# Optimization experiments

Hardware: AMD Instinct MI355X
Metric: run time of the kernel (lower is better)

The kernel has to match this reference:

```python
import jax, jax.numpy as jnp
import numpy as np

N = 50000       # nodes
E = 800000      # edges (avg degree 16)
DIN = 128
DOUT = 128
ALPHA = 0.2     # leaky relu negative slope


def setup_inputs() -> dict:
    key = jax.random.key(0)
    k1, k2, k3, k4, k5 = jax.random.split(key, 5)
    h = jax.random.normal(k1, (N, DIN), dtype=jnp.float32)
    # xavier-normal-ish scaling for params
    W = jax.random.normal(k2, (DIN, DOUT), dtype=jnp.float32) * np.float32(np.sqrt(2.0 / (DIN + DOUT)))
    a = jax.random.normal(k3, (2 * DOUT,), dtype=jnp.float32) * np.float32(np.sqrt(2.0 / (2 * DOUT + 1)))
    src = jax.random.randint(k4, (E,), 0, N, dtype=jnp.int32)
    dst = jax.random.randint(k5, (E,), 0, N, dtype=jnp.int32)
    return {"h": h, "W": W, "a": a, "src": src, "dst": dst}


def reference(h, W, a, src, dst):
    # eval mode: dropout is a no-op (training=False)
    Wh = h @ W                                  # [N, DOUT]
    a_src, a_dst = a[:DOUT], a[DOUT:]
    s = Wh @ a_src                              # [N] per-node src score
    d = Wh @ a_dst                              # [N] per-node dst score
    e = jax.nn.leaky_relu(s[src] + d[dst], negative_slope=ALPHA)  # [E]
    # segment softmax over incoming edges of each dst node
    emax = jax.ops.segment_max(e, dst, num_segments=N)            # [N]
    emax = jnp.where(jnp.isfinite(emax), emax, jnp.float32(0.0))  # isolated nodes
    ex = jnp.exp(e - emax[dst])                                   # [E]
    denom = jax.ops.segment_sum(ex, dst, num_segments=N)          # [N]
    alpha = ex / denom[dst]                                       # [E]
    # weighted scatter-sum of src features into dst nodes
    h_out = jax.ops.segment_sum(alpha[:, None] * Wh[src], dst, num_segments=N)  # [N, DOUT]
    # residual: in_feats == out_feats -> Identity
    return h_out + h
```

## Files before the change

kernel.cpp:

```cpp
#include <hip/hip_runtime.h>
#include <math.h>

#define NN 50000
#define NE 800000
#define DD 128
#define LRELU 0.2f
#define CAP 64

typedef unsigned int uint;

__device__ __forceinline__ uint pack_bf2(float x, float y) {
  uint a = __float_as_uint(x), b = __float_as_uint(y);
  a = (a + 0x7fffu + ((a >> 16) & 1u)) >> 16;
  b = (b + 0x7fffu + ((b >> 16) & 1u)) >> 16;
  return a | (b << 16);
}

__global__ __launch_bounds__(256) void k_gemm(const float* __restrict__ h,
                                              const float* __restrict__ W,
                                              const float* __restrict__ a,
                                              uint* __restrict__ Whb,
                                              float* __restrict__ sv,
                                              float* __restrict__ dv,
                                              int* __restrict__ cnt) {
  __shared__ float hs[32][64];
  __shared__ float Ws[32][128];
  const int tid = threadIdx.x;
  const int brow = blockIdx.x * 64;

  if (tid < 64) {
    int idx = blockIdx.x * 64 + tid;
    if (idx < NN) cnt[idx] = 0;
  }

  const int tx = tid & 15, ty = tid >> 4;
  const int c0 = tx * 4, c1 = 64 + tx * 4;
  float acc[4][8];
#pragma unroll
  for (int r = 0; r < 4; ++r)
#pragma unroll
    for (int j = 0; j < 8; ++j) acc[r][j] = 0.f;

  const int lr = tid >> 2;
  const int lc = (tid & 3) * 8;
  int grow = brow + lr; if (grow >= NN) grow = 0;

  for (int k0 = 0; k0 < DD; k0 += 32) {
    {
      const float4* hp = reinterpret_cast<const float4*>(h + (size_t)grow * DD + k0 + lc);
      float4 v0 = hp[0], v1 = hp[1];
      hs[lc + 0][lr] = v0.x; hs[lc + 1][lr] = v0.y;
      hs[lc + 2][lr] = v0.z; hs[lc + 3][lr] = v0.w;
      hs[lc + 4][lr] = v1.x; hs[lc + 5][lr] = v1.y;
      hs[lc + 6][lr] = v1.z; hs[lc + 7][lr] = v1.w;
    }
#pragma unroll
    for (int i = 0; i < 4; ++i) {
      int f = i * 256 + tid;
      int kk = f >> 5, cc = (f & 31) * 4;
      *reinterpret_cast<float4*>(&Ws[kk][cc]) =
          *reinterpret_cast<const float4*>(W + (size_t)(k0 + kk) * DD + cc);
    }
    __syncthreads();
#pragma unroll
    for (int k = 0; k < 32; ++k) {
      float4 av = *reinterpret_cast<const float4*>(&hs[k][ty * 4]);
      float4 b0 = *reinterpret_cast<const float4*>(&Ws[k][c0]);
      float4 b1 = *reinterpret_cast<const float4*>(&Ws[k][c1]);
      acc[0][0] = fmaf(av.x, b0.x, acc[0][0]); acc[0][1] = fmaf(av.x, b0.y, acc[0][1]);
      acc[0][2] = fmaf(av.x, b0.z, acc[0][2]); acc[0][3] = fmaf(av.x, b0.w, acc[0][3]);
      acc[0][4] = fmaf(av.x, b1.x, acc[0][4]); acc[0][5] = fmaf(av.x, b1.y, acc[0][5]);
      acc[0][6] = fmaf(av.x, b1.z, acc[0][6]); acc[0][7] = fmaf(av.x, b1.w, acc[0][7]);
      acc[1][0] = fmaf(av.y, b0.x, acc[1][0]); acc[1][1] = fmaf(av.y, b0.y, acc[1][1]);
      acc[1][2] = fmaf(av.y, b0.z, acc[1][2]); acc[1][3] = fmaf(av.y, b0.w, acc[1][3]);
      acc[1][4] = fmaf(av.y, b1.x, acc[1][4]); acc[1][5] = fmaf(av.y, b1.y, acc[1][5]);
      acc[1][6] = fmaf(av.y, b1.z, acc[1][6]); acc[1][7] = fmaf(av.y, b1.w, acc[1][7]);
      acc[2][0] = fmaf(av.z, b0.x, acc[2][0]); acc[2][1] = fmaf(av.z, b0.y, acc[2][1]);
      acc[2][2] = fmaf(av.z, b0.z, acc[2][2]); acc[2][3] = fmaf(av.z, b0.w, acc[2][3]);
      acc[2][4] = fmaf(av.z, b1.x, acc[2][4]); acc[2][5] = fmaf(av.z, b1.y, acc[2][5]);
      acc[2][6] = fmaf(av.z, b1.z, acc[2][6]); acc[2][7] = fmaf(av.z, b1.w, acc[2][7]);
      acc[3][0] = fmaf(av.w, b0.x, acc[3][0]); acc[3][1] = fmaf(av.w, b0.y, acc[3][1]);
      acc[3][2] = fmaf(av.w, b0.z, acc[3][2]); acc[3][3] = fmaf(av.w, b0.w, acc[3][3]);
      acc[3][4] = fmaf(av.w, b1.x, acc[3][4]); acc[3][5] = fmaf(av.w, b1.y, acc[3][5]);
      acc[3][6] = fmaf(av.w, b1.z, acc[3][6]); acc[3][7] = fmaf(av.w, b1.w, acc[3][7]);
    }
    __syncthreads();
  }

  float4 as0 = *reinterpret_cast<const float4*>(a + c0);
  float4 as1 = *reinterpret_cast<const float4*>(a + c1);
  float4 ad0 = *reinterpret_cast<const float4*>(a + DD + c0);
  float4 ad1 = *reinterpret_cast<const float4*>(a + DD + c1);
#pragma unroll
  for (int r = 0; r < 4; ++r) {
    int row = brow + ty * 4 + r;
    bool ok = row < NN;
    if (ok) {
      uint2 p0 = make_uint2(pack_bf2(acc[r][0], acc[r][1]), pack_bf2(acc[r][2], acc[r][3]));
      uint2 p1 = make_uint2(pack_bf2(acc[r][4], acc[r][5]), pack_bf2(acc[r][6], acc[r][7]));
      *reinterpret_cast<uint2*>(Whb + (size_t)row * 64 + c0 / 2) = p0;
      *reinterpret_cast<uint2*>(Whb + (size_t)row * 64 + c1 / 2) = p1;
    }
    float ps = acc[r][0] * as0.x + acc[r][1] * as0.y + acc[r][2] * as0.z + acc[r][3] * as0.w
             + acc[r][4] * as1.x + acc[r][5] * as1.y + acc[r][6] * as1.z + acc[r][7] * as1.w;
    float pd = acc[r][0] * ad0.x + acc[r][1] * ad0.y + acc[r][2] * ad0.z + acc[r][3] * ad0.w
             + acc[r][4] * ad1.x + acc[r][5] * ad1.y + acc[r][6] * ad1.z + acc[r][7] * ad1.w;
#pragma unroll
    for (int off = 8; off > 0; off >>= 1) {
      ps += __shfl_xor(ps, off);
      pd += __shfl_xor(pd, off);
    }
    if (tx == 0 && ok) { sv[row] = ps; dv[row] = pd; }
  }
}

__global__ __launch_bounds__(256) void k_fill(const int* __restrict__ src,
                                              const int* __restrict__ dst,
                                              int* __restrict__ cnt,
                                              int* __restrict__ srcs) {
  int i = blockIdx.x * 256 + threadIdx.x;
  if (i >= NE) return;
  int d = dst[i];
  int p = atomicAdd(&cnt[d], 1);
  if (p < CAP) srcs[(size_t)d * CAP + p] = src[i];
}

__global__ __launch_bounds__(256) void k_node(const float* __restrict__ h,
                                              const uint* __restrict__ Whb,
                                              const float* __restrict__ sv,
                                              const float* __restrict__ dv,
                                              const int* __restrict__ cnt,
                                              const int* __restrict__ srcs,
                                              float* __restrict__ out) {
  int wid = (blockIdx.x * 256 + threadIdx.x) >> 6;
  if (wid >= NN) return;
  wid = __builtin_amdgcn_readfirstlane(wid);
  const int lane = threadIdx.x & 63;

  float2 hrow = reinterpret_cast<const float2*>(h + (size_t)wid * DD)[lane];
  int deg = cnt[wid];
  deg = deg < CAP ? deg : CAP;
  float2* o2 = reinterpret_cast<float2*>(out + (size_t)wid * DD);
  if (deg == 0) { o2[lane] = hrow; return; }

  const int* bucket = srcs + (size_t)wid * CAP;
  const float dvn = dv[wid];

  float m = -INFINITY;
  for (int k = lane; k < deg; k += 64) {
    float ev = sv[bucket[k]] + dvn;
    ev = ev > 0.f ? ev : LRELU * ev;
    m = fmaxf(m, ev);
  }
#pragma unroll
  for (int off = 32; off > 0; off >>= 1) m = fmaxf(m, __shfl_xor(m, off));

  float2 accA = make_float2(0.f, 0.f);
  float2 accB = make_float2(0.f, 0.f);
  float den = 0.f;
  int k = 0;
  for (; k + 2 <= deg; k += 2) {
    int s0 = bucket[k], s1 = bucket[k + 1];
    float e0 = sv[s0] + dvn; e0 = e0 > 0.f ? e0 : LRELU * e0;
    float e1 = sv[s1] + dvn; e1 = e1 > 0.f ? e1 : LRELU * e1;
    float x0 = __expf(e0 - m), x1 = __expf(e1 - m);
    den += x0 + x1;
    uint u0 = Whb[(size_t)s0 * 64 + lane];
    uint u1 = Whb[(size_t)s1 * 64 + lane];
    accA.x = fmaf(x0, __uint_as_float(u0 << 16), accA.x);
    accA.y = fmaf(x0, __uint_as_float(u0 & 0xffff0000u), accA.y);
    accB.x = fmaf(x1, __uint_as_float(u1 << 16), accB.x);
    accB.y = fmaf(x1, __uint_as_float(u1 & 0xffff0000u), accB.y);
  }
  if (k < deg) {
    int s0 = bucket[k];
    float e0 = sv[s0] + dvn; e0 = e0 > 0.f ? e0 : LRELU * e0;
    float x0 = __expf(e0 - m);
    den += x0;
    uint u0 = Whb[(size_t)s0 * 64 + lane];
    accA.x = fmaf(x0, __uint_as_float(u0 << 16), accA.x);
    accA.y = fmaf(x0, __uint_as_float(u0 & 0xffff0000u), accA.y);
  }
  float inv = 1.0f / den;
  o2[lane] = make_float2(hrow.x + (accA.x + accB.x) * inv,
                         hrow.y + (accA.y + accB.y) * inv);
}

extern "C" void kernel_launch(void* const* d_in, const int* in_sizes, int n_in,
                              void* d_out, int out_size, void* d_ws, size_t ws_size,
                              hipStream_t stream) {
  const float* h = (const float*)d_in[0];
  const float* W = (const float*)d_in[1];
  const float* a = (const float*)d_in[2];
  const int* src = (const int*)d_in[3];
  const int* dst = (const int*)d_in[4];
  float* out = (float*)d_out;

  char* ws = (char*)d_ws;
  uint*  Whb = (uint*) (ws);
  float* sv  = (float*)(ws + 12800000);
  float* dv  = (float*)(ws + 13000000);
  int*   cnt = (int*)  (ws + 13200000);
  int*   srcs= (int*)  (ws + 13400000);

  hipLaunchKernelGGL(k_gemm, dim3((NN + 63) / 64), dim3(256), 0, stream,
                     h, W, a, Whb, sv, dv, cnt);
  hipLaunchKernelGGL(k_fill, dim3((NE + 255) / 256), dim3(256), 0, stream,
                     src, dst, cnt, srcs);
  hipLaunchKernelGGL(k_node, dim3((NN + 3) / 4), dim3(256), 0, stream,
                     h, Whb, sv, dv, cnt, srcs, out);
}
```

Measured before the change: 201.1 us.

## Precompute edge exp weights in fill and partition nodes by XCD slice

The fill kernel now computes each edge's LeakyReLU score and its exponential, and stores (src, weight) pairs in the per-node buckets. The node kernel therefore no longer does the gather-based max pass or the exp work. Both the fill and node kernels split destination nodes into 8 slices keyed on blockIdx&7, so that the atomics, bucket writes and later reads for a node tend to stay within one XCD's L2. In exchange, every fill block scans its edge range 8 times, the bucket entries double in size, and dropping the max subtraction risks exp overflow on inputs with large scores.

```diff
diff --git a/kernel.cpp b/kernel.cpp
--- a/kernel.cpp
+++ b/kernel.cpp
@@ -6,6 +6,7 @@
 #define DD 128
 #define LRELU 0.2f
 #define CAP 64
+#define SLICE 6256
 
 typedef unsigned int uint;
 
@@ -116,24 +117,34 @@
 
 __global__ __launch_bounds__(256) void k_fill(const int* __restrict__ src,
                                               const int* __restrict__ dst,
+                                              const float* __restrict__ sv,
+                                              const float* __restrict__ dv,
                                               int* __restrict__ cnt,
-                                              int* __restrict__ srcs) {
-  int i = blockIdx.x * 256 + threadIdx.x;
-  if (i >= NE) return;
-  int d = dst[i];
-  int p = atomicAdd(&cnt[d], 1);
-  if (p < CAP) srcs[(size_t)d * CAP + p] = src[i];
+                                              uint2* __restrict__ entries) {
+  const int xcd = blockIdx.x & 7;
+  const int e0 = (blockIdx.x >> 3) * 3125;
+  const int e1 = e0 + 3125;
+  for (int i = e0 + threadIdx.x; i < e1; i += 256) {
+    int d = dst[i];
+    if (d / SLICE != xcd) continue;
+    int s = src[i];
+    float ev = sv[s] + dv[d];
+    ev = ev > 0.f ? ev : LRELU * ev;
+    float x = __expf(ev);
+    int p = atomicAdd(&cnt[d], 1);
+    if (p < CAP) entries[(size_t)d * CAP + p] = make_uint2((uint)s, __float_as_uint(x));
+  }
 }
 
 __global__ __launch_bounds__(256) void k_node(const float* __restrict__ h,
                                               const uint* __restrict__ Whb,
-                                              const float* __restrict__ sv,
-                                              const float* __restrict__ dv,
                                               const int* __restrict__ cnt,
-                                              const int* __restrict__ srcs,
+                                              const uint2* __restrict__ entries,
                                               float* __restrict__ out) {
-  int wid = (blockIdx.x * 256 + threadIdx.x) >> 6;
-  if (wid >= NN) return;
+  const int sl = blockIdx.x & 7;
+  int wid = sl * SLICE + (blockIdx.x >> 3) * 4 + (threadIdx.x >> 6);
+  const int lim = min(NN, (sl + 1) * SLICE);
+  if (wid >= lim) return;
   wid = __builtin_amdgcn_readfirstlane(wid);
   const int lane = threadIdx.x & 63;
 
@@ -143,41 +154,27 @@
   float2* o2 = reinterpret_cast<float2*>(out + (size_t)wid * DD);
   if (deg == 0) { o2[lane] = hrow; return; }
 
-  const int* bucket = srcs + (size_t)wid * CAP;
-  const float dvn = dv[wid];
-
-  float m = -INFINITY;
-  for (int k = lane; k < deg; k += 64) {
-    float ev = sv[bucket[k]] + dvn;
-    ev = ev > 0.f ? ev : LRELU * ev;
-    m = fmaxf(m, ev);
-  }
-#pragma unroll
-  for (int off = 32; off > 0; off >>= 1) m = fmaxf(m, __shfl_xor(m, off));
-
+  const uint2* bucket = entries + (size_t)wid * CAP;
   float2 accA = make_float2(0.f, 0.f);
   float2 accB = make_float2(0.f, 0.f);
   float den = 0.f;
   int k = 0;
   for (; k + 2 <= deg; k += 2) {
-    int s0 = bucket[k], s1 = bucket[k + 1];
-    float e0 = sv[s0] + dvn; e0 = e0 > 0.f ? e0 : LRELU * e0;
-    float e1 = sv[s1] + dvn; e1 = e1 > 0.f ? e1 : LRELU * e1;
-    float x0 = __expf(e0 - m), x1 = __expf(e1 - m);
+    uint2 q0 = bucket[k], q1 = bucket[k + 1];
+    float x0 = __uint_as_float(q0.y), x1 = __uint_as_float(q1.y);
     den += x0 + x1;
-    uint u0 = Whb[(size_t)s0 * 64 + lane];
-    uint u1 = Whb[(size_t)s1 * 64 + lane];
+    uint u0 = Whb[(size_t)q0.x * 64 + lane];
+    uint u1 = Whb[(size_t)q1.x * 64 + lane];
     accA.x = fmaf(x0, __uint_as_float(u0 << 16), accA.x);
     accA.y = fmaf(x0, __uint_as_float(u0 & 0xffff0000u), accA.y);
     accB.x = fmaf(x1, __uint_as_float(u1 << 16), accB.x);
     accB.y = fmaf(x1, __uint_as_float(u1 & 0xffff0000u), accB.y);
   }
   if (k < deg) {
-    int s0 = bucket[k];
-    float e0 = sv[s0] + dvn; e0 = e0 > 0.f ? e0 : LRELU * e0;
-    float x0 = __expf(e0 - m);
+    uint2 q0 = bucket[k];
+    float x0 = __uint_as_float(q0.y);
     den += x0;
-    uint u0 = Whb[(size_t)s0 * 64 + lane];
+    uint u0 = Whb[(size_t)q0.x * 64 + lane];
     accA.x = fmaf(x0, __uint_as_float(u0 << 16), accA.x);
     accA.y = fmaf(x0, __uint_as_float(u0 & 0xffff0000u), accA.y);
   }
@@ -197,16 +194,16 @@
   float* out = (float*)d_out;
 
   char* ws = (char*)d_ws;
-  uint*  Whb = (uint*) (ws);
-  float* sv  = (float*)(ws + 12800000);
-  float* dv  = (float*)(ws + 13000000);
-  int*   cnt = (int*)  (ws + 13200000);
-  int*   srcs= (int*)  (ws + 13400000);
+  uint*  Whb     = (uint*) (ws);
+  float* sv      = (float*)(ws + 12800000);
+  float* dv      = (float*)(ws + 13000000);
+  int*   cnt     = (int*)  (ws + 13200000);
+  uint2* entries = (uint2*)(ws + 13400000);
 
   hipLaunchKernelGGL(k_gemm, dim3((NN + 63) / 64), dim3(256), 0, stream,
                      h, W, a, Whb, sv, dv, cnt);
-  hipLaunchKernelGGL(k_fill, dim3((NE + 255) / 256), dim3(256), 0, stream,
-                     src, dst, cnt, srcs);
-  hipLaunchKernelGGL(k_node, dim3((NN + 3) / 4), dim3(256), 0, stream,
-                     h, Whb, sv, dv, cnt, srcs, out);
-}
+  hipLaunchKernelGGL(k_fill, dim3(2048), dim3(256), 0, stream,
+                     src, dst, sv, dv, cnt, entries);
+  hipLaunchKernelGGL(k_node, dim3(8 * ((SLICE + 3) / 4)), dim3(256), 0, stream,
+                     h, Whb, cnt, entries, out);
+}
```

After: 185.5 us. 1.08x faster.
